# Performance work log

Measured on AMD Instinct MI355X. Metric: run time of the kernel, lower is better.

The kernel has to match this reference:

```python
import jax, jax.numpy as jnp
import numpy as np

NUM_CLASSES = 80
STRIDES = (8, 16, 32)


def _decode(p, stride):
    # p: [B, 5+C, H, W] raw head -> [B, HW, 5+C] decoded (xy in px, wh=exp*stride)
    B, C, H, W = p.shape
    ys, xs = jnp.meshgrid(jnp.arange(H), jnp.arange(W), indexing='ij')
    grid = jnp.stack([xs, ys], -1).reshape(H * W, 2).astype(p.dtype)
    out = p.reshape(B, C, H * W).transpose(0, 2, 1)
    xy = (out[..., :2] + grid) * stride
    wh = jnp.exp(out[..., 2:4]) * stride
    out = jnp.concatenate([xy, wh, out[..., 4:]], -1)
    es = jnp.full((H * W,), float(stride), p.dtype)
    return out, grid[:, 0], grid[:, 1], es


def _pairwise_iou(gt, pr):
    # gt [G,4] cxcywh, pr [A,4] -> [G,A]
    gt_tl = gt[:, None, :2] - gt[:, None, 2:] * 0.5
    gt_br = gt[:, None, :2] + gt[:, None, 2:] * 0.5
    pr_tl = pr[None, :, :2] - pr[None, :, 2:] * 0.5
    pr_br = pr[None, :, :2] + pr[None, :, 2:] * 0.5
    tl = jnp.maximum(gt_tl, pr_tl)
    br = jnp.minimum(gt_br, pr_br)
    en = jnp.all(tl < br, -1).astype(gt.dtype)
    inter = jnp.prod(br - tl, -1) * en
    a_gt = jnp.prod(gt[:, 2:], -1)[:, None]
    a_pr = jnp.prod(pr[:, 2:], -1)[None, :]
    return inter / (a_gt + a_pr - inter + 1e-16)


def _assign(gt_boxes, gt_cls, bbox, clsp, objp, xg, yg, es):
    # SimOTA assignment for one image (all fixed-shape; non-candidate anchors
    # are masked out via huge cost instead of boolean gather).
    G = gt_boxes.shape[0]
    xc = (xg + 0.5) * es  # [A] anchor centers
    yc = (yg + 0.5) * es
    gl = gt_boxes[:, 0:1] - 0.5 * gt_boxes[:, 2:3]
    gr = gt_boxes[:, 0:1] + 0.5 * gt_boxes[:, 2:3]
    gt_ = gt_boxes[:, 1:2] - 0.5 * gt_boxes[:, 3:4]
    gb = gt_boxes[:, 1:2] + 0.5 * gt_boxes[:, 3:4]
    in_box = (xc[None] > gl) & (xc[None] < gr) & (yc[None] > gt_) & (yc[None] < gb)  # [G,A]
    r = 2.5 * es[None]
    in_ctr = ((xc[None] > gt_boxes[:, 0:1] - r) & (xc[None] < gt_boxes[:, 0:1] + r)
              & (yc[None] > gt_boxes[:, 1:2] - r) & (yc[None] < gt_boxes[:, 1:2] + r))
    fg_cand = jnp.any(in_box, 0) | jnp.any(in_ctr, 0)  # [A]
    in_both = in_box & in_ctr  # [G,A]

    ious = _pairwise_iou(gt_boxes, bbox)  # [G,A]
    ious_m = jnp.where(fg_cand[None, :], ious, 0.0)
    iou_cost = -jnp.log(ious_m + 1e-8)

    # pairwise cls BCE cost: bce(sqrt(sigmoid(cls)*sigmoid(obj)), onehot(gt)).sum(-1)
    p = jnp.sqrt(jax.nn.sigmoid(clsp) * jax.nn.sigmoid(objp[:, None]))  # [A,C]
    lp = jnp.maximum(jnp.log(p), -100.0)
    l1p = jnp.maximum(jnp.log1p(-p), -100.0)
    t = jax.nn.one_hot(gt_cls, NUM_CLASSES, dtype=p.dtype)  # [G,C]
    cls_cost = -(jnp.einsum('ac,gc->ga', lp - l1p, t) + jnp.sum(l1p, -1)[None, :])

    cost = (cls_cost + 3.0 * iou_cost
            + 1e5 * (~in_both).astype(p.dtype)
            + 1e9 * (~fg_cand)[None, :].astype(p.dtype))

    # dynamic-k: k_g = clamp(sum(top10 ious), min=1)
    topk_ious, _ = jax.lax.top_k(ious_m, 10)
    dyn_k = jnp.clip(topk_ious.sum(-1).astype(jnp.int32), 1, None)  # [G]
    rank = jnp.argsort(jnp.argsort(cost, axis=1), axis=1)  # rank of each anchor per gt
    matching = (rank < dyn_k[:, None]) & fg_cand[None, :]  # [G,A]
    # resolve anchors matched to multiple gts: keep min-cost gt
    multi = matching.sum(0) > 1
    best = jnp.argmin(cost, 0)
    matching = jnp.where(multi[None, :], jnp.arange(G)[:, None] == best[None, :], matching)

    fg = jnp.any(matching, 0)  # [A]
    matched_gt = jnp.argmax(matching, 0)  # [A]
    pred_iou = jnp.sum(matching * ious, 0)  # [A]
    matched_cls = gt_cls[matched_gt]
    return fg, matched_gt, pred_iou, matched_cls


def _giou_loss(b, g):
    tl = jnp.maximum(b[..., :2] - b[..., 2:] * 0.5, g[..., :2] - g[..., 2:] * 0.5)
    br = jnp.minimum(b[..., :2] + b[..., 2:] * 0.5, g[..., :2] + g[..., 2:] * 0.5)
    area_b = jnp.prod(b[..., 2:], -1)
    area_g = jnp.prod(g[..., 2:], -1)
    en = jnp.all(tl < br, -1).astype(b.dtype)
    inter = jnp.prod(br - tl, -1) * en
    union = area_b + area_g - inter
    iou = inter / (union + 1e-16)
    ctl = jnp.minimum(b[..., :2] - b[..., 2:] * 0.5, g[..., :2] - g[..., 2:] * 0.5)
    cbr = jnp.maximum(b[..., :2] + b[..., 2:] * 0.5, g[..., :2] + g[..., 2:] * 0.5)
    area_c = jnp.maximum(jnp.prod(cbr - ctl, -1), 1e-16)
    giou = iou - (area_c - union) / area_c
    return 1.0 - jnp.clip(giou, -1.0, 1.0)


def _bce_logits(x, t):
    return jnp.maximum(x, 0.0) - x * t + jnp.log1p(jnp.exp(-jnp.abs(x)))


def _forward(p8, p16, p32, labels):
    outs, xo, yo, eo = [], [], [], []
    for p, s in zip((p8, p16, p32), STRIDES):
        o, x, y, e = _decode(p, s)
        outs.append(o); xo.append(x); yo.append(y); eo.append(e)
    outputs = jnp.concatenate(outs, 1)  # [B, A, 5+C]
    xg = jnp.concatenate(xo); yg = jnp.concatenate(yo); es = jnp.concatenate(eo)

    bbox = outputs[..., :4]
    obj = outputs[..., 4]
    cls = outputs[..., 5:]
    gt_boxes = labels[..., :4]
    gt_cls = labels[..., 4].astype(jnp.int32)

    # assignment runs under no_grad in torch
    det = jax.lax.stop_gradient(outputs)
    fg, matched_gt, pred_iou, matched_cls = jax.vmap(
        lambda gb, gc, o: _assign(gb, gc, o[..., :4], o[..., 5:], o[..., 4], xg, yg, es)
    )(gt_boxes, gt_cls, det)

    fgf = fg.astype(outputs.dtype)  # [B,A]
    reg_t = jnp.take_along_axis(gt_boxes, matched_gt[..., None], axis=1)  # [B,A,4]
    cls_t = (jax.nn.one_hot(matched_cls, NUM_CLASSES, dtype=outputs.dtype)
             * pred_iou[..., None] * fgf[..., None])

    loss_iou = jnp.sum(_giou_loss(bbox, reg_t) * fgf)
    loss_obj = jnp.sum(_bce_logits(obj, fgf))
    loss_cls = jnp.sum(_bce_logits(cls, cls_t) * fgf[..., None])
    num_fg = jnp.maximum(jnp.sum(fgf), 1.0)
    return (5.0 * loss_iou + loss_obj + loss_cls) / num_fg


def setup_inputs() -> dict:
    key = jax.random.key(0)
    k1, k2, k3, k4, k5, k6 = jax.random.split(key, 6)
    B, NGT = 32, 20
    p8 = jax.random.normal(k1, (B, 5 + NUM_CLASSES, 80, 80), dtype=jnp.float32)
    p16 = jax.random.normal(k2, (B, 5 + NUM_CLASSES, 40, 40), dtype=jnp.float32)
    p32 = jax.random.normal(k3, (B, 5 + NUM_CLASSES, 20, 20), dtype=jnp.float32)
    cxy = jax.random.uniform(k4, (B, NGT, 2), dtype=jnp.float32, minval=32.0, maxval=608.0)
    wh = jax.random.uniform(k5, (B, NGT, 2), dtype=jnp.float32, minval=16.0, maxval=128.0)
    cls = jax.random.randint(k6, (B, NGT, 1), 0, NUM_CLASSES).astype(jnp.float32)
    labels = jnp.concatenate([cxy, wh, cls], -1)
    return {"p8": p8, "p16": p16, "p32": p32, "labels": labels}


def reference(p8, p16, p32, labels):
    return _forward(p8, p16, p32, labels)
```

## Files before the change

kernel.cpp:

```cpp
#include <hip/hip_runtime.h>
#include <cstdint>
#include <cstddef>

#define NA 8400
#define NAP 8448
#define NB 32
#define NG 20
#define NCL 80
#define NBLK 33

__device__ __forceinline__ float frcp(float x) { return __builtin_amdgcn_rcpf(x); }
__device__ __forceinline__ float bce0(float x) {
  return fmaxf(x, 0.0f) + __logf(1.0f + __expf(-fabsf(x)));
}

__device__ __forceinline__ void anchor_info(int a, const float* p8, const float* p16,
                                            const float* p32, int b, const float*& base,
                                            int& hw, int& HW, int& xg, int& yg, float& fs) {
  if (a < 6400)      { hw = a;        HW = 6400; xg = hw % 80; yg = hw / 80; fs = 8.f;
                       base = p8  + (size_t)b * 85 * 6400; }
  else if (a < 8000) { hw = a - 6400; HW = 1600; xg = hw % 40; yg = hw / 40; fs = 16.f;
                       base = p16 + (size_t)b * 85 * 1600; }
  else               { hw = a - 8000; HW = 400;  xg = hw % 20; yg = hw / 20; fs = 32.f;
                       base = p32 + (size_t)b * 85 * 400; }
}

__device__ __forceinline__ float iou_raw(float gx, float gy, float gw, float gh, float4 p) {
  float gtlx = gx - gw * 0.5f, gtly = gy - gh * 0.5f;
  float gbrx = gx + gw * 0.5f, gbry = gy + gh * 0.5f;
  float ptlx = p.x - p.z * 0.5f, ptly = p.y - p.w * 0.5f;
  float pbrx = p.x + p.z * 0.5f, pbry = p.y + p.w * 0.5f;
  float tlx = fmaxf(gtlx, ptlx), tly = fmaxf(gtly, ptly);
  float brx = fminf(gbrx, pbrx), bry = fminf(gbry, pbry);
  float inter = ((tlx < brx) && (tly < bry)) ? (brx - tlx) * (bry - tly) : 0.0f;
  float ag = gw * gh, ap = p.z * p.w;
  return inter * frcp(ag + ap - inter + 1e-16f);
}

__device__ __forceinline__ float giou_loss(float4 bb, float gx, float gy, float gw, float gh) {
  float btlx = bb.x - bb.z * 0.5f, btly = bb.y - bb.w * 0.5f;
  float bbrx = bb.x + bb.z * 0.5f, bbry = bb.y + bb.w * 0.5f;
  float gtlx = gx - gw * 0.5f, gtly = gy - gh * 0.5f;
  float gbrx = gx + gw * 0.5f, gbry = gy + gh * 0.5f;
  float tlx = fmaxf(btlx, gtlx), tly = fmaxf(btly, gtly);
  float brx = fminf(bbrx, gbrx), bry = fminf(bbry, gbry);
  float area_b = bb.z * bb.w, area_g = gw * gh;
  float inter = ((tlx < brx) && (tly < bry)) ? (brx - tlx) * (bry - tly) : 0.0f;
  float uni = area_b + area_g - inter;
  float iou = inter / (uni + 1e-16f);
  float ctlx = fminf(btlx, gtlx), ctly = fminf(btly, gtly);
  float cbrx = fmaxf(bbrx, gbrx), cbry = fmaxf(bbry, gbry);
  float area_c = fmaxf((cbrx - ctlx) * (cbry - ctly), 1e-16f);
  float giou = iou - (area_c - uni) / area_c;
  giou = fminf(fmaxf(giou, -1.0f), 1.0f);
  return 1.0f - giou;
}

__global__ __launch_bounds__(256) void k1(const float* __restrict__ p8,
                                          const float* __restrict__ p16,
                                          const float* __restrict__ p32,
                                          const float* __restrict__ labels,
                                          int* __restrict__ n_fg_cnt,
                                          int* __restrict__ fg_list,
                                          unsigned int* __restrict__ am_c,
                                          float4* __restrict__ bbox_c,
                                          float* __restrict__ lso_c,
                                          unsigned int* __restrict__ match_c,
                                          float* __restrict__ blk_obj) {
  __shared__ float s_gt[NG * 4];
  __shared__ unsigned int s_wcnt[4];
  __shared__ float s_part[4];
  __shared__ unsigned int s_base;
  int blk = blockIdx.x, b = blockIdx.y, tid = threadIdx.x, lane = tid & 63, wid = tid >> 6;

  if (tid < NG) {
    s_gt[tid * 4 + 0] = labels[((size_t)b * NG + tid) * 5 + 0];
    s_gt[tid * 4 + 1] = labels[((size_t)b * NG + tid) * 5 + 1];
    s_gt[tid * 4 + 2] = labels[((size_t)b * NG + tid) * 5 + 2];
    s_gt[tid * 4 + 3] = labels[((size_t)b * NG + tid) * 5 + 3];
  }
  __syncthreads();

  int a = blk * 256 + tid;
  match_c[(size_t)b * NAP + a] = 0u;

  bool fg = false;
  unsigned int msk = 0u;
  float bce_obj = 0.0f, obj = 0.0f;
  const float* base = nullptr; int hw = 0, HW = 0, xg = 0, yg = 0; float fs = 8.f;
  if (a < NA) {
    anchor_info(a, p8, p16, p32, b, base, hw, HW, xg, yg, fs);
    obj = base[4 * HW + hw];
    bce_obj = bce0(obj);
    float xc = ((float)xg + 0.5f) * fs;
    float yc = ((float)yg + 0.5f) * fs;
    float r = 2.5f * fs;
#pragma unroll
    for (int g = 0; g < NG; ++g) {
      float gx = s_gt[g * 4 + 0], gy = s_gt[g * 4 + 1];
      float gw = s_gt[g * 4 + 2], gh = s_gt[g * 4 + 3];
      bool inb = (xc > gx - 0.5f * gw) && (xc < gx + 0.5f * gw) &&
                 (yc > gy - 0.5f * gh) && (yc < gy + 0.5f * gh);
      bool inc = (xc > gx - r) && (xc < gx + r) && (yc > gy - r) && (yc < gy + r);
      fg = fg || inb || inc;
      if (inb && inc) msk |= (1u << g);
    }
  }

  unsigned long long bm = __ballot(fg);
#pragma unroll
  for (int off = 32; off; off >>= 1) bce_obj += __shfl_down(bce_obj, off, 64);
  if (lane == 0) { s_wcnt[wid] = (unsigned int)__popcll(bm); s_part[wid] = bce_obj; }
  __syncthreads();
  if (tid == 0) {
    unsigned int cnt = s_wcnt[0] + s_wcnt[1] + s_wcnt[2] + s_wcnt[3];
    s_base = cnt ? (unsigned int)atomicAdd(&n_fg_cnt[b], (int)cnt) : 0u;
    blk_obj[b * NBLK + blk] = s_part[0] + s_part[1] + s_part[2] + s_part[3];
  }
  __syncthreads();

  if (!fg) return;
  unsigned int pos = s_base;
  for (int w = 0; w < wid; ++w) pos += s_wcnt[w];
  pos += (unsigned int)__popcll(bm & ((1ull << lane) - 1ull));
  size_t bo = (size_t)b * NAP;
  int ci = (int)pos;
  fg_list[bo + ci] = a;
  am_c[bo + ci] = msk;

  float v0 = base[hw];
  float v1 = base[HW + hw];
  float v2 = base[2 * HW + hw];
  float v3 = base[3 * HW + hw];
  bbox_c[bo + ci] = make_float4((v0 + (float)xg) * fs, (v1 + (float)yg) * fs,
                                __expf(v2) * fs, __expf(v3) * fs);
  float uo = __logf(1.0f + __expf(-fabsf(obj)));
  lso_c[bo + ci] = fminf(obj, 0.0f) - uo;
}

__global__ __launch_bounds__(256) void k23(const float* __restrict__ p8,
                                           const float* __restrict__ p16,
                                           const float* __restrict__ p32,
                                           const float* __restrict__ labels,
                                           const int* __restrict__ fg_list,
                                           const int* __restrict__ n_fg,
                                           const float* __restrict__ lso_c,
                                           const unsigned int* __restrict__ am_c,
                                           const float4* __restrict__ bbox_c,
                                           float* __restrict__ sb_c,
                                           float* __restrict__ cost_tbl,
                                           float* __restrict__ iou_tbl) {
  __shared__ float s_gt[NG * 4];
  __shared__ int   s_gcls[NG];
  __shared__ float s_sl[8][33];
  __shared__ float s_sb[8][33];
  __shared__ float s_slr[32];
  int b = blockIdx.y, tid = threadIdx.x;
  int part = tid >> 5, cl = tid & 31;

  if (tid < NG) {
    s_gt[tid * 4 + 0] = labels[((size_t)b * NG + tid) * 5 + 0];
    s_gt[tid * 4 + 1] = labels[((size_t)b * NG + tid) * 5 + 1];
    s_gt[tid * 4 + 2] = labels[((size_t)b * NG + tid) * 5 + 2];
    s_gt[tid * 4 + 3] = labels[((size_t)b * NG + tid) * 5 + 3];
    s_gcls[tid] = (int)labels[((size_t)b * NG + tid) * 5 + 4];
  }
  __syncthreads();

  int n = n_fg[b];
  size_t bo = (size_t)b * NAP;

  for (int base_ci = blockIdx.x * 32; base_ci < n; base_ci += gridDim.x * 32) {
    int ci = base_ci + cl;
    bool act = ci < n;
    const float* base = nullptr; int hw = 0, HW = 0, xg, yg; float fs;
    float lso = 0.0f, sl = 0.0f, sb = 0.0f;
    if (act) {
      int a = fg_list[bo + ci];
      lso = lso_c[bo + ci];
      anchor_info(a, p8, p16, p32, b, base, hw, HW, xg, yg, fs);
      const float* cb = base + (size_t)(5 + part * 10) * HW + hw;
      float xs[10];
#pragma unroll
      for (int j = 0; j < 10; ++j) xs[j] = cb[(size_t)j * HW];
#pragma unroll
      for (int j = 0; j < 10; ++j) {
        float x = xs[j];
        float u = __logf(1.0f + __expf(-fabsf(x)));
        sb += fmaxf(x, 0.0f) + u;
        float lsx = fminf(x, 0.0f) - u;
        float lpr = 0.5f * (lsx + lso);
        float p   = __expf(lpr);
        sl += fmaxf(__logf(1.0f - p), -100.0f);
      }
    }
    s_sl[part][cl] = sl;
    s_sb[part][cl] = sb;
    __syncthreads();
    if (tid < 32) {
      float tsl = 0.0f, tsb = 0.0f;
#pragma unroll
      for (int q = 0; q < 8; ++q) { tsl += s_sl[q][tid]; tsb += s_sb[q][tid]; }
      s_slr[tid] = tsl;
      if (base_ci + tid < n) sb_c[bo + base_ci + tid] = tsb;
    }
    __syncthreads();
    if (act) {
      float slr = s_slr[cl];
      unsigned int am = am_c[bo + ci];
      float4 pb = bbox_c[bo + ci];
#pragma unroll
      for (int gg = 0; gg < 3; ++gg) {
        int g = part + (gg << 3);
        if (g < NG) {
          int cg = s_gcls[g];
          float x = base[(size_t)(5 + cg) * HW + hw];
          float u = __logf(1.0f + __expf(-fabsf(x)));
          float lsx = fminf(x, 0.0f) - u;
          float lpr = 0.5f * (lsx + lso);
          float p   = __expf(lpr);
          float l1p = fmaxf(__logf(1.0f - p), -100.0f);
          float wv  = fmaxf(lpr, -100.0f) - l1p;
          float iou = iou_raw(s_gt[g * 4 + 0], s_gt[g * 4 + 1],
                              s_gt[g * 4 + 2], s_gt[g * 4 + 3], pb);
          float cst = -(wv + slr) - 3.0f * __logf(iou + 1e-8f);
          if (!((am >> g) & 1u)) cst += 100000.0f;
          size_t row = ((size_t)b * NG + g) * NAP;
          cost_tbl[row + ci] = cst;
          iou_tbl[row + ci]  = iou;
        }
      }
    }
    __syncthreads();
  }
}

__global__ __launch_bounds__(256) void kBCD(const float* __restrict__ p8,
                                            const float* __restrict__ p16,
                                            const float* __restrict__ p32,
                                            const float* __restrict__ labels,
                                            const float* __restrict__ cost_tbl,
                                            const float* __restrict__ iou_tbl,
                                            const int* __restrict__ n_fg,
                                            unsigned int* __restrict__ match_c,
                                            const int* __restrict__ fg_list,
                                            const float4* __restrict__ bbox_c,
                                            const float* __restrict__ sb_c,
                                            const float* __restrict__ blk_obj,
                                            float* __restrict__ accum,
                                            int* __restrict__ done_g,
                                            int* __restrict__ done_img,
                                            float* __restrict__ out) {
  __shared__ float s_wt[4 * 10];
  __shared__ float s_wc[4 * 10];
  __shared__ int   s_wi[4 * 10];
  __shared__ int   s_flag;
  __shared__ float s_gt[NG * 5];
  __shared__ float s_red[16];

  int g = blockIdx.x, b = blockIdx.y, tid = threadIdx.x;
  int lane = tid & 63, wid = tid >> 6;
  int n = n_fg[b];
  size_t bo = (size_t)b * NAP;
  const float* __restrict__ cg = cost_tbl + ((size_t)b * NG + g) * NAP;
  const float* __restrict__ ig = iou_tbl  + ((size_t)b * NG + g) * NAP;

  float t10[10];
  float c10v[10];
  int   c10i[10];
#pragma unroll
  for (int j = 0; j < 10; ++j) { t10[j] = 0.0f; c10v[j] = 3.4e38f; c10i[j] = 0x7fffffff; }

  for (int ci = tid; ci < n; ci += 256) {
    float iou = ig[ci];
    float cst = cg[ci];
    if (iou > t10[9]) {
      t10[9] = iou;
#pragma unroll
      for (int q = 9; q > 0; --q) {
        if (t10[q] > t10[q - 1]) { float t = t10[q]; t10[q] = t10[q - 1]; t10[q - 1] = t; }
        else break;
      }
    }
    if (cst < c10v[9] || (cst == c10v[9] && ci < c10i[9])) {
      c10v[9] = cst; c10i[9] = ci;
#pragma unroll
      for (int q = 9; q > 0; --q) {
        if (c10v[q] < c10v[q - 1] ||
            (c10v[q] == c10v[q - 1] && c10i[q] < c10i[q - 1])) {
          float tv = c10v[q]; c10v[q] = c10v[q - 1]; c10v[q - 1] = tv;
          int   ti = c10i[q]; c10i[q] = c10i[q - 1]; c10i[q - 1] = ti;
        } else break;
      }
    }
  }

  for (int r = 0; r < 10; ++r) {
    float v = t10[0];
    float bv = v;
    float cv = c10v[0]; int cix = c10i[0];
    float cbv = cv;     int cbi = cix;
#pragma unroll
    for (int off = 32; off; off >>= 1) {
      bv = fmaxf(bv, __shfl_down(bv, off, 64));
      float ov = __shfl_down(cbv, off, 64);
      int   oi = __shfl_down(cbi, off, 64);
      if (ov < cbv || (ov == cbv && oi < cbi)) { cbv = ov; cbi = oi; }
    }
    bv  = __shfl(bv, 0, 64);
    cbv = __shfl(cbv, 0, 64);
    cbi = __shfl(cbi, 0, 64);
    unsigned long long won = __ballot(v == bv);
    if (lane == __ffsll(won) - 1) {
#pragma unroll
      for (int q = 0; q < 9; ++q) t10[q] = t10[q + 1];
      t10[9] = -1.0f;
    }
    if (cv == cbv && cix == cbi) {
#pragma unroll
      for (int q = 0; q < 9; ++q) { c10v[q] = c10v[q + 1]; c10i[q] = c10i[q + 1]; }
      c10v[9] = 3.4e38f; c10i[9] = 0x7fffffff;
    }
    if (lane == 0) {
      s_wt[wid * 10 + r] = bv;
      s_wc[wid * 10 + r] = cbv;
      s_wi[wid * 10 + r] = cbi;
    }
  }
  __syncthreads();

  if (tid == 0) {
    int p0 = 0, p1 = 0, p2 = 0, p3 = 0;
    float s = 0.0f;
    for (int r = 0; r < 10; ++r) {
      float v0 = (p0 < 10) ? s_wt[p0]      : -2.0f;
      float v1 = (p1 < 10) ? s_wt[10 + p1] : -2.0f;
      float v2 = (p2 < 10) ? s_wt[20 + p2] : -2.0f;
      float v3 = (p3 < 10) ? s_wt[30 + p3] : -2.0f;
      float m = fmaxf(fmaxf(v0, v1), fmaxf(v2, v3));
      s += m;
      if (m == v0) ++p0; else if (m == v1) ++p1; else if (m == v2) ++p2; else ++p3;
    }
    int k = (int)s;
    if (k < 1) k = 1;
    int q[4] = {0, 0, 0, 0};
    for (int it = 0; it < k; ++it) {
      float bv = 3.3e38f; int bi = 0x7fffffff; int sel = -1;
#pragma unroll
      for (int w = 0; w < 4; ++w) {
        if (q[w] < 10) {
          float v = s_wc[w * 10 + q[w]];
          int   i = s_wi[w * 10 + q[w]];
          if (v < bv || (v == bv && i < bi)) { bv = v; bi = i; sel = w; }
        }
      }
      if (sel < 0 || bv >= 1e37f) break;
      atomicOr(&match_c[bo + bi], 1u << g);
      ++q[sel];
    }
    __threadfence();
    s_flag = (atomicAdd(&done_g[b], 1) == NG - 1) ? 1 : 0;
  }
  __syncthreads();
  if (!s_flag) return;

  if (tid < NG * 5) s_gt[tid] = labels[(size_t)b * NG * 5 + tid];
  __syncthreads();

  float li = 0.0f, oe = 0.0f, lc = 0.0f, nf = 0.0f;
  for (int ci = tid; ci < n; ci += 256) {
    unsigned int m = atomicOr(&match_c[bo + ci], 0u);
    if (m == 0u) continue;
    int mg;
    if (m & (m - 1)) {
      float bestc = 3.4e38f; mg = 0;
#pragma unroll 4
      for (int gq = 0; gq < NG; ++gq) {
        float cst = cost_tbl[((size_t)b * NG + gq) * NAP + ci];
        if (cst < bestc) { bestc = cst; mg = gq; }
      }
    } else {
      mg = __ffs(m) - 1;
    }
    int a = fg_list[bo + ci];
    const float* base; int hw, HW, xg, yg; float fs;
    anchor_info(a, p8, p16, p32, b, base, hw, HW, xg, yg, fs);
    float4 pb = bbox_c[bo + ci];
    float gx = s_gt[mg * 5], gy = s_gt[mg * 5 + 1];
    float gw = s_gt[mg * 5 + 2], gh = s_gt[mg * 5 + 3];
    int cgq = (int)s_gt[mg * 5 + 4];
    float piou = iou_tbl[((size_t)b * NG + mg) * NAP + ci];
    li += giou_loss(pb, gx, gy, gw, gh);
    float xcls = base[(size_t)(5 + cgq) * HW + hw];
    lc += sb_c[bo + ci] - xcls * piou;
    oe += base[4 * HW + hw];
    nf += 1.0f;
  }

  float vals[4] = {li, oe, lc, nf};
#pragma unroll
  for (int q2 = 0; q2 < 4; ++q2) {
#pragma unroll
    for (int off = 32; off; off >>= 1) vals[q2] += __shfl_down(vals[q2], off, 64);
  }
  if ((tid & 63) == 0) {
    int w = tid >> 6;
    s_red[w * 4 + 0] = vals[0];
    s_red[w * 4 + 1] = vals[1];
    s_red[w * 4 + 2] = vals[2];
    s_red[w * 4 + 3] = vals[3];
  }
  __syncthreads();
  if (tid < 4) {
    const int slot[4] = {0, 2, 3, 4};
    float s = s_red[tid] + s_red[4 + tid] + s_red[8 + tid] + s_red[12 + tid];
    atomicAdd(&accum[slot[tid]], s);
  }

  if (tid == 0) {
    __threadfence();
    s_flag = (atomicAdd(done_img, 1) == NB - 1) ? 1 : 0;
  }
  __syncthreads();
  if (!s_flag) return;

  float s = 0.0f;
  for (int i = tid; i < NB * NBLK; i += 256) s += blk_obj[i];
#pragma unroll
  for (int off = 32; off; off >>= 1) s += __shfl_down(s, off, 64);
  if ((tid & 63) == 0) s_red[tid >> 6] = s;
  __syncthreads();
  if (tid == 0) {
    float obj_base = s_red[0] + s_red[1] + s_red[2] + s_red[3];
    float loss_iou = atomicAdd(&accum[0], 0.0f);
    float oex      = atomicAdd(&accum[2], 0.0f);
    float loss_cls = atomicAdd(&accum[3], 0.0f);
    float num_fg   = atomicAdd(&accum[4], 0.0f);
    float loss_obj = obj_base - oex;
    out[0] = (5.0f * loss_iou + loss_obj + loss_cls) / fmaxf(num_fg, 1.0f);
  }
}

extern "C" void kernel_launch(void* const* d_in, const int* in_sizes, int n_in,
                              void* d_out, int out_size, void* d_ws, size_t ws_size,
                              hipStream_t stream) {
  const float* p8     = (const float*)d_in[0];
  const float* p16    = (const float*)d_in[1];
  const float* p32    = (const float*)d_in[2];
  const float* labels = (const float*)d_in[3];
  float* out = (float*)d_out;

  const size_t BAP = (size_t)NB * NAP;
  char* w = (char*)d_ws;
  float4*       bbox_c   = (float4*)w;
  float*        cost_tbl = (float*)(w + BAP * 16);
  float*        iou_tbl  = cost_tbl + (size_t)NB * NG * NAP;
  char*         w2       = (char*)(iou_tbl + (size_t)NB * NG * NAP);
  int*          fg_list  = (int*)(w2);
  unsigned int* match_c  = (unsigned int*)(w2 + BAP * 4);
  float*        sb_c     = (float*)(w2 + BAP * 8);
  float*        lso_c    = (float*)(w2 + BAP * 12);
  unsigned int* am_c     = (unsigned int*)(w2 + BAP * 16);
  char*         w3       = w2 + BAP * 20;
  int*          n_fg     = (int*)w3;
  float*        accum    = (float*)(w3 + 128);
  int*          done_g   = (int*)(w3 + 256);
  int*          done_img = (int*)(w3 + 384);
  float*        blk_obj  = (float*)(w3 + 512);

  hipMemsetAsync(w3, 0, 512, stream);

  k1<<<dim3(NBLK, NB), dim3(256), 0, stream>>>(p8, p16, p32, labels, n_fg, fg_list, am_c,
                                               bbox_c, lso_c, match_c, blk_obj);
  k23<<<dim3(NBLK, NB), dim3(256), 0, stream>>>(p8, p16, p32, labels, fg_list, n_fg, lso_c,
                                                am_c, bbox_c, sb_c, cost_tbl, iou_tbl);
  kBCD<<<dim3(NG, NB), dim3(256), 0, stream>>>(p8, p16, p32, labels, cost_tbl, iou_tbl,
                                               n_fg, match_c, fg_list, bbox_c, sb_c,
                                               blk_obj, accum, done_g, done_img, out);
}
```

Baseline: 183.5 us.

## Split SimOTA top-k matching into partitioned kernels and interleave cost/iou tables

New measurement: 207.4 us. 13.1% more time.

```diff
diff --git a/kernel.cpp b/kernel.cpp
--- a/kernel.cpp
+++ b/kernel.cpp
@@ -8,6 +8,7 @@
 #define NG 20
 #define NCL 80
 #define NBLK 33
+#define PSPL 4
 
 __device__ __forceinline__ float frcp(float x) { return __builtin_amdgcn_rcpf(x); }
 __device__ __forceinline__ float bce0(float x) {
@@ -148,8 +149,7 @@
                                            const unsigned int* __restrict__ am_c,
                                            const float4* __restrict__ bbox_c,
                                            float* __restrict__ sb_c,
-                                           float* __restrict__ cost_tbl,
-                                           float* __restrict__ iou_tbl) {
+                                           float2* __restrict__ ct_tbl) {
   __shared__ float s_gt[NG * 4];
   __shared__ int   s_gcls[NG];
   __shared__ float s_sl[8][33];
@@ -225,9 +225,7 @@
                               s_gt[g * 4 + 2], s_gt[g * 4 + 3], pb);
           float cst = -(wv + slr) - 3.0f * __logf(iou + 1e-8f);
           if (!((am >> g) & 1u)) cst += 100000.0f;
-          size_t row = ((size_t)b * NG + g) * NAP;
-          cost_tbl[row + ci] = cst;
-          iou_tbl[row + ci]  = iou;
+          ct_tbl[((size_t)b * NG + g) * NAP + ci] = make_float2(cst, iou);
         }
       }
     }
@@ -235,35 +233,18 @@
   }
 }
 
-__global__ __launch_bounds__(256) void kBCD(const float* __restrict__ p8,
-                                            const float* __restrict__ p16,
-                                            const float* __restrict__ p32,
-                                            const float* __restrict__ labels,
-                                            const float* __restrict__ cost_tbl,
-                                            const float* __restrict__ iou_tbl,
-                                            const int* __restrict__ n_fg,
-                                            unsigned int* __restrict__ match_c,
-                                            const int* __restrict__ fg_list,
-                                            const float4* __restrict__ bbox_c,
-                                            const float* __restrict__ sb_c,
-                                            const float* __restrict__ blk_obj,
-                                            float* __restrict__ accum,
-                                            int* __restrict__ done_g,
-                                            int* __restrict__ done_img,
-                                            float* __restrict__ out) {
+__global__ __launch_bounds__(256) void kBC(const float2* __restrict__ ct_tbl,
+                                           const int* __restrict__ n_fg,
+                                           float* __restrict__ scr_iou,
+                                           float* __restrict__ scr_cst,
+                                           int* __restrict__ scr_ci) {
   __shared__ float s_wt[4 * 10];
   __shared__ float s_wc[4 * 10];
   __shared__ int   s_wi[4 * 10];
-  __shared__ int   s_flag;
-  __shared__ float s_gt[NG * 5];
-  __shared__ float s_red[16];
-
-  int g = blockIdx.x, b = blockIdx.y, tid = threadIdx.x;
-  int lane = tid & 63, wid = tid >> 6;
+  int p = blockIdx.x, g = blockIdx.y, b = blockIdx.z;
+  int tid = threadIdx.x, lane = tid & 63, wid = tid >> 6;
   int n = n_fg[b];
-  size_t bo = (size_t)b * NAP;
-  const float* __restrict__ cg = cost_tbl + ((size_t)b * NG + g) * NAP;
-  const float* __restrict__ ig = iou_tbl  + ((size_t)b * NG + g) * NAP;
+  const float2* __restrict__ row = ct_tbl + ((size_t)b * NG + g) * NAP;
 
   float t10[10];
   float c10v[10];
@@ -271,9 +252,9 @@
 #pragma unroll
   for (int j = 0; j < 10; ++j) { t10[j] = 0.0f; c10v[j] = 3.4e38f; c10i[j] = 0x7fffffff; }
 
-  for (int ci = tid; ci < n; ci += 256) {
-    float iou = ig[ci];
-    float cst = cg[ci];
+  for (int ci = p * 256 + tid; ci < n; ci += PSPL * 256) {
+    float2 e = row[ci];
+    float cst = e.x, iou = e.y;
     if (iou > t10[9]) {
       t10[9] = iou;
 #pragma unroll
@@ -330,71 +311,138 @@
   __syncthreads();
 
   if (tid == 0) {
+    int obase = (((b * NG + g) * PSPL) + p) * 10;
     int p0 = 0, p1 = 0, p2 = 0, p3 = 0;
-    float s = 0.0f;
     for (int r = 0; r < 10; ++r) {
       float v0 = (p0 < 10) ? s_wt[p0]      : -2.0f;
       float v1 = (p1 < 10) ? s_wt[10 + p1] : -2.0f;
       float v2 = (p2 < 10) ? s_wt[20 + p2] : -2.0f;
       float v3 = (p3 < 10) ? s_wt[30 + p3] : -2.0f;
       float m = fmaxf(fmaxf(v0, v1), fmaxf(v2, v3));
-      s += m;
+      scr_iou[obase + r] = m;
       if (m == v0) ++p0; else if (m == v1) ++p1; else if (m == v2) ++p2; else ++p3;
     }
-    int k = (int)s;
-    if (k < 1) k = 1;
     int q[4] = {0, 0, 0, 0};
-    for (int it = 0; it < k; ++it) {
-      float bv = 3.3e38f; int bi = 0x7fffffff; int sel = -1;
+    for (int r = 0; r < 10; ++r) {
+      float bv = 0.0f; int bi = 0; int sel = -1;
 #pragma unroll
       for (int w = 0; w < 4; ++w) {
         if (q[w] < 10) {
           float v = s_wc[w * 10 + q[w]];
           int   i = s_wi[w * 10 + q[w]];
-          if (v < bv || (v == bv && i < bi)) { bv = v; bi = i; sel = w; }
+          if (sel < 0 || v < bv || (v == bv && i < bi)) { bv = v; bi = i; sel = w; }
         }
       }
-      if (sel < 0 || bv >= 1e37f) break;
-      atomicOr(&match_c[bo + bi], 1u << g);
+      scr_cst[obase + r] = bv;
+      scr_ci[obase + r]  = bi;
       ++q[sel];
     }
-    __threadfence();
-    s_flag = (atomicAdd(&done_g[b], 1) == NG - 1) ? 1 : 0;
-  }
-  __syncthreads();
-  if (!s_flag) return;
+  }
+}
+
+__global__ __launch_bounds__(64) void kM(const float* __restrict__ scr_iou,
+                                         const float* __restrict__ scr_cst,
+                                         const int* __restrict__ scr_ci,
+                                         unsigned int* __restrict__ match_c) {
+  int g = blockIdx.x, b = blockIdx.y, lane = threadIdx.x;
+  int bg = b * NG + g;
+  float v;
+  float cv; int cix;
+  if (lane < PSPL * 10) {
+    v   = scr_iou[bg * (PSPL * 10) + lane];
+    cv  = scr_cst[bg * (PSPL * 10) + lane];
+    cix = scr_ci [bg * (PSPL * 10) + lane];
+  } else {
+    v = -1.0f; cv = 3.4e38f; cix = 0x7fffffff;
+  }
+
+  float s = 0.0f;
+  for (int r = 0; r < 10; ++r) {
+    float bv = v;
+#pragma unroll
+    for (int off = 32; off; off >>= 1) bv = fmaxf(bv, __shfl_down(bv, off, 64));
+    bv = __shfl(bv, 0, 64);
+    s += bv;
+    unsigned long long won = __ballot(v == bv);
+    if (lane == __ffsll(won) - 1) v = -1.0f;
+  }
+  int k = (int)s;
+  if (k < 1) k = 1;
+
+  size_t bo = (size_t)b * NAP;
+  for (int it = 0; it < k; ++it) {
+    float cbv = cv; int cbi = cix;
+#pragma unroll
+    for (int off = 32; off; off >>= 1) {
+      float ov = __shfl_down(cbv, off, 64);
+      int   oi = __shfl_down(cbi, off, 64);
+      if (ov < cbv || (ov == cbv && oi < cbi)) { cbv = ov; cbi = oi; }
+    }
+    cbv = __shfl(cbv, 0, 64);
+    cbi = __shfl(cbi, 0, 64);
+    if (cbv >= 1e37f) break;
+    unsigned long long won = __ballot(cv == cbv && cix == cbi);
+    if (lane == __ffsll(won) - 1) {
+      atomicOr(&match_c[bo + cbi], 1u << g);
+      cv = 3.4e38f; cix = 0x7fffffff;
+    }
+  }
+}
+
+__global__ __launch_bounds__(256) void kD(const float* __restrict__ p8,
+                                          const float* __restrict__ p16,
+                                          const float* __restrict__ p32,
+                                          const float* __restrict__ labels,
+                                          const float2* __restrict__ ct_tbl,
+                                          const int* __restrict__ n_fg,
+                                          const unsigned int* __restrict__ match_c,
+                                          const int* __restrict__ fg_list,
+                                          const float4* __restrict__ bbox_c,
+                                          const float* __restrict__ sb_c,
+                                          const float* __restrict__ blk_obj,
+                                          float* __restrict__ accum,
+                                          int* __restrict__ done,
+                                          float* __restrict__ out) {
+  __shared__ float s_gt[NG * 5];
+  __shared__ float s_red[16];
+  __shared__ int s_flag;
+  int b = blockIdx.y, tid = threadIdx.x;
+  int n = n_fg[b];
+  size_t bo = (size_t)b * NAP;
 
   if (tid < NG * 5) s_gt[tid] = labels[(size_t)b * NG * 5 + tid];
   __syncthreads();
 
   float li = 0.0f, oe = 0.0f, lc = 0.0f, nf = 0.0f;
-  for (int ci = tid; ci < n; ci += 256) {
-    unsigned int m = atomicOr(&match_c[bo + ci], 0u);
-    if (m == 0u) continue;
-    int mg;
-    if (m & (m - 1)) {
-      float bestc = 3.4e38f; mg = 0;
+  int ci = blockIdx.x * 256 + tid;
+  if (ci < n) {
+    unsigned int m = match_c[bo + ci];
+    if (m != 0u) {
+      int mg;
+      if (m & (m - 1)) {
+        float bestc = 3.4e38f; mg = 0;
 #pragma unroll 4
-      for (int gq = 0; gq < NG; ++gq) {
-        float cst = cost_tbl[((size_t)b * NG + gq) * NAP + ci];
-        if (cst < bestc) { bestc = cst; mg = gq; }
+        for (int gq = 0; gq < NG; ++gq) {
+          float cst = ct_tbl[((size_t)b * NG + gq) * NAP + ci].x;
+          if (cst < bestc) { bestc = cst; mg = gq; }
+        }
+      } else {
+        mg = __ffs(m) - 1;
       }
-    } else {
-      mg = __ffs(m) - 1;
-    }
-    int a = fg_list[bo + ci];
-    const float* base; int hw, HW, xg, yg; float fs;
-    anchor_info(a, p8, p16, p32, b, base, hw, HW, xg, yg, fs);
-    float4 pb = bbox_c[bo + ci];
-    float gx = s_gt[mg * 5], gy = s_gt[mg * 5 + 1];
-    float gw = s_gt[mg * 5 + 2], gh = s_gt[mg * 5 + 3];
-    int cgq = (int)s_gt[mg * 5 + 4];
-    float piou = iou_tbl[((size_t)b * NG + mg) * NAP + ci];
-    li += giou_loss(pb, gx, gy, gw, gh);
-    float xcls = base[(size_t)(5 + cgq) * HW + hw];
-    lc += sb_c[bo + ci] - xcls * piou;
-    oe += base[4 * HW + hw];
-    nf += 1.0f;
+      int a = fg_list[bo + ci];
+      const float* base; int hw, HW, xg, yg; float fs;
+      anchor_info(a, p8, p16, p32, b, base, hw, HW, xg, yg, fs);
+      float4 pb = bbox_c[bo + ci];
+      float gx = s_gt[mg * 5], gy = s_gt[mg * 5 + 1];
+      float gw = s_gt[mg * 5 + 2], gh = s_gt[mg * 5 + 3];
+      int cgq = (int)s_gt[mg * 5 + 4];
+      float piou = ct_tbl[((size_t)b * NG + mg) * NAP + ci].y;
+      li = giou_loss(pb, gx, gy, gw, gh);
+      float xcls = base[(size_t)(5 + cgq) * HW + hw];
+      lc = sb_c[bo + ci] - xcls * piou;
+      oe = base[4 * HW + hw];
+      nf = 1.0f;
+    }
   }
 
   float vals[4] = {li, oe, lc, nf};
@@ -403,7 +451,8 @@
 #pragma unroll
     for (int off = 32; off; off >>= 1) vals[q2] += __shfl_down(vals[q2], off, 64);
   }
-  if ((tid & 63) == 0) {
+  int lane = tid & 63;
+  if (lane == 0) {
     int w = tid >> 6;
     s_red[w * 4 + 0] = vals[0];
     s_red[w * 4 + 1] = vals[1];
@@ -414,12 +463,13 @@
   if (tid < 4) {
     const int slot[4] = {0, 2, 3, 4};
     float s = s_red[tid] + s_red[4 + tid] + s_red[8 + tid] + s_red[12 + tid];
-    atomicAdd(&accum[slot[tid]], s);
-  }
+    if (s != 0.0f) atomicAdd(&accum[slot[tid]], s);
+  }
+  __syncthreads();
 
   if (tid == 0) {
     __threadfence();
-    s_flag = (atomicAdd(done_img, 1) == NB - 1) ? 1 : 0;
+    s_flag = (atomicAdd(done, 1) == NBLK * NB - 1) ? 1 : 0;
   }
   __syncthreads();
   if (!s_flag) return;
@@ -453,9 +503,8 @@
   const size_t BAP = (size_t)NB * NAP;
   char* w = (char*)d_ws;
   float4*       bbox_c   = (float4*)w;
-  float*        cost_tbl = (float*)(w + BAP * 16);
-  float*        iou_tbl  = cost_tbl + (size_t)NB * NG * NAP;
-  char*         w2       = (char*)(iou_tbl + (size_t)NB * NG * NAP);
+  float2*       ct_tbl   = (float2*)(w + BAP * 16);
+  char*         w2       = (char*)ct_tbl + (size_t)NB * NG * NAP * 8;
   int*          fg_list  = (int*)(w2);
   unsigned int* match_c  = (unsigned int*)(w2 + BAP * 4);
   float*        sb_c     = (float*)(w2 + BAP * 8);
@@ -464,17 +513,22 @@
   char*         w3       = w2 + BAP * 20;
   int*          n_fg     = (int*)w3;
   float*        accum    = (float*)(w3 + 128);
-  int*          done_g   = (int*)(w3 + 256);
-  int*          done_img = (int*)(w3 + 384);
+  int*          done     = (int*)(w3 + 384);
   float*        blk_obj  = (float*)(w3 + 512);
+  char*         scr      = w3 + 8192;
+  float*        scr_iou  = (float*)scr;
+  float*        scr_cst  = (float*)(scr + 102400);
+  int*          scr_ci   = (int*)  (scr + 204800);
 
   hipMemsetAsync(w3, 0, 512, stream);
 
-  k1<<<dim3(NBLK, NB), dim3(256), 0, stream>>>(p8, p16, p32, labels, n_fg, fg_list, am_c,
-                                               bbox_c, lso_c, match_c, blk_obj);
+  k1 <<<dim3(NBLK, NB), dim3(256), 0, stream>>>(p8, p16, p32, labels, n_fg, fg_list, am_c,
+                                                bbox_c, lso_c, match_c, blk_obj);
   k23<<<dim3(NBLK, NB), dim3(256), 0, stream>>>(p8, p16, p32, labels, fg_list, n_fg, lso_c,
-                                                am_c, bbox_c, sb_c, cost_tbl, iou_tbl);
-  kBCD<<<dim3(NG, NB), dim3(256), 0, stream>>>(p8, p16, p32, labels, cost_tbl, iou_tbl,
-                                               n_fg, match_c, fg_list, bbox_c, sb_c,
-                                               blk_obj, accum, done_g, done_img, out);
-}
+                                                am_c, bbox_c, sb_c, ct_tbl);
+  kBC<<<dim3(PSPL, NG, NB), dim3(256), 0, stream>>>(ct_tbl, n_fg, scr_iou, scr_cst, scr_ci);
+  kM <<<dim3(NG, NB), dim3(64), 0, stream>>>(scr_iou, scr_cst, scr_ci, match_c);
+  kD <<<dim3(NBLK, NB), dim3(256), 0, stream>>>(p8, p16, p32, labels, ct_tbl, n_fg, match_c,
+                                                fg_list, bbox_c, sb_c, blk_obj, accum,
+                                                done, out);
+}
```

## Fuse candidate and class-sum kernels; recompute per-GT cost instead of storing tables

Applied to the files above, without the earlier changes.

New measurement: 188.3 us. +2.6%, slower.

```diff
diff --git a/kernel.cpp b/kernel.cpp
--- a/kernel.cpp
+++ b/kernel.cpp
@@ -35,6 +35,24 @@
   float inter = ((tlx < brx) && (tly < bry)) ? (brx - tlx) * (bry - tly) : 0.0f;
   float ag = gw * gh, ap = p.z * p.w;
   return inter * frcp(ag + ap - inter + 1e-16f);
+}
+
+__device__ __forceinline__ float cost_for(float gx, float gy, float gw, float gh, int cg,
+                                          int g, unsigned int am, float lso, float slr,
+                                          const float* base, int hw, int HW, float4 pb,
+                                          float& iou_out) {
+  float x = base[(size_t)(5 + cg) * HW + hw];
+  float u = __logf(1.0f + __expf(-fabsf(x)));
+  float lsx = fminf(x, 0.0f) - u;
+  float lpr = 0.5f * (lsx + lso);
+  float p   = __expf(lpr);
+  float l1p = fmaxf(__logf(1.0f - p), -100.0f);
+  float wv  = fmaxf(lpr, -100.0f) - l1p;
+  float iou = iou_raw(gx, gy, gw, gh, pb);
+  iou_out = iou;
+  float cst = -(wv + slr) - 3.0f * __logf(iou + 1e-8f);
+  if (!((am >> g) & 1u)) cst += 100000.0f;
+  return cst;
 }
 
 __device__ __forceinline__ float giou_loss(float4 bb, float gx, float gy, float gw, float gh) {
@@ -56,22 +74,29 @@
   return 1.0f - giou;
 }
 
-__global__ __launch_bounds__(256) void k1(const float* __restrict__ p8,
+__global__ __launch_bounds__(256) void kA(const float* __restrict__ p8,
                                           const float* __restrict__ p16,
                                           const float* __restrict__ p32,
                                           const float* __restrict__ labels,
                                           int* __restrict__ n_fg_cnt,
-                                          int* __restrict__ fg_list,
-                                          unsigned int* __restrict__ am_c,
+                                          float4* __restrict__ meta_c,
                                           float4* __restrict__ bbox_c,
-                                          float* __restrict__ lso_c,
+                                          float* __restrict__ sb_c,
                                           unsigned int* __restrict__ match_c,
                                           float* __restrict__ blk_obj) {
   __shared__ float s_gt[NG * 4];
+  __shared__ int   s_a[256];
+  __shared__ unsigned int s_m[256];
+  __shared__ float s_lso[256];
+  __shared__ float s_sl[8][33];
+  __shared__ float s_sbv[8][33];
   __shared__ unsigned int s_wcnt[4];
   __shared__ float s_part[4];
   __shared__ unsigned int s_base;
+  __shared__ int s_cnt;
+
   int blk = blockIdx.x, b = blockIdx.y, tid = threadIdx.x, lane = tid & 63, wid = tid >> 6;
+  size_t bo = (size_t)b * NAP;
 
   if (tid < NG) {
     s_gt[tid * 4 + 0] = labels[((size_t)b * NG + tid) * 5 + 0];
@@ -82,8 +107,7 @@
   __syncthreads();
 
   int a = blk * 256 + tid;
-  match_c[(size_t)b * NAP + a] = 0u;
-
+  match_c[bo + a] = 0u;
   bool fg = false;
   unsigned int msk = 0u;
   float bce_obj = 0.0f, obj = 0.0f;
@@ -114,75 +138,44 @@
   __syncthreads();
   if (tid == 0) {
     unsigned int cnt = s_wcnt[0] + s_wcnt[1] + s_wcnt[2] + s_wcnt[3];
+    s_cnt = (int)cnt;
     s_base = cnt ? (unsigned int)atomicAdd(&n_fg_cnt[b], (int)cnt) : 0u;
     blk_obj[b * NBLK + blk] = s_part[0] + s_part[1] + s_part[2] + s_part[3];
   }
   __syncthreads();
 
-  if (!fg) return;
-  unsigned int pos = s_base;
-  for (int w = 0; w < wid; ++w) pos += s_wcnt[w];
-  pos += (unsigned int)__popcll(bm & ((1ull << lane) - 1ull));
-  size_t bo = (size_t)b * NAP;
-  int ci = (int)pos;
-  fg_list[bo + ci] = a;
-  am_c[bo + ci] = msk;
-
-  float v0 = base[hw];
-  float v1 = base[HW + hw];
-  float v2 = base[2 * HW + hw];
-  float v3 = base[3 * HW + hw];
-  bbox_c[bo + ci] = make_float4((v0 + (float)xg) * fs, (v1 + (float)yg) * fs,
-                                __expf(v2) * fs, __expf(v3) * fs);
-  float uo = __logf(1.0f + __expf(-fabsf(obj)));
-  lso_c[bo + ci] = fminf(obj, 0.0f) - uo;
-}
-
-__global__ __launch_bounds__(256) void k23(const float* __restrict__ p8,
-                                           const float* __restrict__ p16,
-                                           const float* __restrict__ p32,
-                                           const float* __restrict__ labels,
-                                           const int* __restrict__ fg_list,
-                                           const int* __restrict__ n_fg,
-                                           const float* __restrict__ lso_c,
-                                           const unsigned int* __restrict__ am_c,
-                                           const float4* __restrict__ bbox_c,
-                                           float* __restrict__ sb_c,
-                                           float* __restrict__ cost_tbl,
-                                           float* __restrict__ iou_tbl) {
-  __shared__ float s_gt[NG * 4];
-  __shared__ int   s_gcls[NG];
-  __shared__ float s_sl[8][33];
-  __shared__ float s_sb[8][33];
-  __shared__ float s_slr[32];
-  int b = blockIdx.y, tid = threadIdx.x;
+  if (fg) {
+    unsigned int li = 0;
+    for (int w = 0; w < wid; ++w) li += s_wcnt[w];
+    li += (unsigned int)__popcll(bm & ((1ull << lane) - 1ull));
+    float v0 = base[hw];
+    float v1 = base[HW + hw];
+    float v2 = base[2 * HW + hw];
+    float v3 = base[3 * HW + hw];
+    float4 bb4 = make_float4((v0 + (float)xg) * fs, (v1 + (float)yg) * fs,
+                             __expf(v2) * fs, __expf(v3) * fs);
+    float uo = __logf(1.0f + __expf(-fabsf(obj)));
+    float lso = fminf(obj, 0.0f) - uo;
+    s_a[li] = a; s_m[li] = msk; s_lso[li] = lso;
+    bbox_c[bo + s_base + li] = bb4;
+  }
+  __syncthreads();
+
+  int cnt = s_cnt;
   int part = tid >> 5, cl = tid & 31;
-
-  if (tid < NG) {
-    s_gt[tid * 4 + 0] = labels[((size_t)b * NG + tid) * 5 + 0];
-    s_gt[tid * 4 + 1] = labels[((size_t)b * NG + tid) * 5 + 1];
-    s_gt[tid * 4 + 2] = labels[((size_t)b * NG + tid) * 5 + 2];
-    s_gt[tid * 4 + 3] = labels[((size_t)b * NG + tid) * 5 + 3];
-    s_gcls[tid] = (int)labels[((size_t)b * NG + tid) * 5 + 4];
-  }
-  __syncthreads();
-
-  int n = n_fg[b];
-  size_t bo = (size_t)b * NAP;
-
-  for (int base_ci = blockIdx.x * 32; base_ci < n; base_ci += gridDim.x * 32) {
-    int ci = base_ci + cl;
-    bool act = ci < n;
-    const float* base = nullptr; int hw = 0, HW = 0, xg, yg; float fs;
-    float lso = 0.0f, sl = 0.0f, sb = 0.0f;
+  for (int t0 = 0; t0 < cnt; t0 += 32) {
+    int idx = t0 + cl;
+    bool act = idx < cnt;
+    float sl = 0.0f, sb = 0.0f;
     if (act) {
-      int a = fg_list[bo + ci];
-      lso = lso_c[bo + ci];
-      anchor_info(a, p8, p16, p32, b, base, hw, HW, xg, yg, fs);
-      const float* cb = base + (size_t)(5 + part * 10) * HW + hw;
+      int a2 = s_a[idx];
+      float lso = s_lso[idx];
+      const float* base2; int hw2, HW2, xg2, yg2; float fs2;
+      anchor_info(a2, p8, p16, p32, b, base2, hw2, HW2, xg2, yg2, fs2);
+      const float* cb = base2 + (size_t)(5 + part * 10) * HW2 + hw2;
       float xs[10];
 #pragma unroll
-      for (int j = 0; j < 10; ++j) xs[j] = cb[(size_t)j * HW];
+      for (int j = 0; j < 10; ++j) xs[j] = cb[(size_t)j * HW2];
 #pragma unroll
       for (int j = 0; j < 10; ++j) {
         float x = xs[j];
@@ -195,75 +188,57 @@
       }
     }
     s_sl[part][cl] = sl;
-    s_sb[part][cl] = sb;
+    s_sbv[part][cl] = sb;
     __syncthreads();
     if (tid < 32) {
-      float tsl = 0.0f, tsb = 0.0f;
-#pragma unroll
-      for (int q = 0; q < 8; ++q) { tsl += s_sl[q][tid]; tsb += s_sb[q][tid]; }
-      s_slr[tid] = tsl;
-      if (base_ci + tid < n) sb_c[bo + base_ci + tid] = tsb;
+      int idx2 = t0 + tid;
+      if (idx2 < cnt) {
+        float tsl = 0.0f, tsb = 0.0f;
+#pragma unroll
+        for (int q = 0; q < 8; ++q) { tsl += s_sl[q][tid]; tsb += s_sbv[q][tid]; }
+        int ci = (int)s_base + idx2;
+        sb_c[bo + ci] = tsb;
+        meta_c[bo + ci] = make_float4(s_lso[idx2], tsl,
+                                      __uint_as_float(s_m[idx2]),
+                                      __int_as_float(s_a[idx2]));
+      }
     }
     __syncthreads();
-    if (act) {
-      float slr = s_slr[cl];
-      unsigned int am = am_c[bo + ci];
-      float4 pb = bbox_c[bo + ci];
-#pragma unroll
-      for (int gg = 0; gg < 3; ++gg) {
-        int g = part + (gg << 3);
-        if (g < NG) {
-          int cg = s_gcls[g];
-          float x = base[(size_t)(5 + cg) * HW + hw];
-          float u = __logf(1.0f + __expf(-fabsf(x)));
-          float lsx = fminf(x, 0.0f) - u;
-          float lpr = 0.5f * (lsx + lso);
-          float p   = __expf(lpr);
-          float l1p = fmaxf(__logf(1.0f - p), -100.0f);
-          float wv  = fmaxf(lpr, -100.0f) - l1p;
-          float iou = iou_raw(s_gt[g * 4 + 0], s_gt[g * 4 + 1],
-                              s_gt[g * 4 + 2], s_gt[g * 4 + 3], pb);
-          float cst = -(wv + slr) - 3.0f * __logf(iou + 1e-8f);
-          if (!((am >> g) & 1u)) cst += 100000.0f;
-          size_t row = ((size_t)b * NG + g) * NAP;
-          cost_tbl[row + ci] = cst;
-          iou_tbl[row + ci]  = iou;
-        }
-      }
-    }
-    __syncthreads();
-  }
-}
-
-__global__ __launch_bounds__(256) void kBCD(const float* __restrict__ p8,
-                                            const float* __restrict__ p16,
-                                            const float* __restrict__ p32,
-                                            const float* __restrict__ labels,
-                                            const float* __restrict__ cost_tbl,
-                                            const float* __restrict__ iou_tbl,
-                                            const int* __restrict__ n_fg,
-                                            unsigned int* __restrict__ match_c,
-                                            const int* __restrict__ fg_list,
-                                            const float4* __restrict__ bbox_c,
-                                            const float* __restrict__ sb_c,
-                                            const float* __restrict__ blk_obj,
-                                            float* __restrict__ accum,
-                                            int* __restrict__ done_g,
-                                            int* __restrict__ done_img,
-                                            float* __restrict__ out) {
+  }
+}
+
+__global__ __launch_bounds__(256) void kBG(const float* __restrict__ p8,
+                                           const float* __restrict__ p16,
+                                           const float* __restrict__ p32,
+                                           const float* __restrict__ labels,
+                                           const int* __restrict__ n_fg,
+                                           const float4* __restrict__ meta_c,
+                                           const float4* __restrict__ bbox_c,
+                                           const float* __restrict__ sb_c,
+                                           unsigned int* __restrict__ match_c,
+                                           const float* __restrict__ blk_obj,
+                                           float* __restrict__ accum,
+                                           int* __restrict__ done_g,
+                                           int* __restrict__ done_img,
+                                           float* __restrict__ out) {
+  __shared__ float s_gt[NG * 5];
   __shared__ float s_wt[4 * 10];
   __shared__ float s_wc[4 * 10];
   __shared__ int   s_wi[4 * 10];
+  __shared__ float s_red[16];
   __shared__ int   s_flag;
-  __shared__ float s_gt[NG * 5];
-  __shared__ float s_red[16];
 
   int g = blockIdx.x, b = blockIdx.y, tid = threadIdx.x;
   int lane = tid & 63, wid = tid >> 6;
   int n = n_fg[b];
   size_t bo = (size_t)b * NAP;
-  const float* __restrict__ cg = cost_tbl + ((size_t)b * NG + g) * NAP;
-  const float* __restrict__ ig = iou_tbl  + ((size_t)b * NG + g) * NAP;
+
+  if (tid < NG * 5) s_gt[tid] = labels[(size_t)b * NG * 5 + tid];
+  __syncthreads();
+
+  float ggx = s_gt[g * 5], ggy = s_gt[g * 5 + 1];
+  float ggw = s_gt[g * 5 + 2], ggh = s_gt[g * 5 + 3];
+  int   gcg = (int)s_gt[g * 5 + 4];
 
   float t10[10];
   float c10v[10];
@@ -272,8 +247,15 @@
   for (int j = 0; j < 10; ++j) { t10[j] = 0.0f; c10v[j] = 3.4e38f; c10i[j] = 0x7fffffff; }
 
   for (int ci = tid; ci < n; ci += 256) {
-    float iou = ig[ci];
-    float cst = cg[ci];
+    float4 me = meta_c[bo + ci];
+    float lso = me.x, slr = me.y;
+    unsigned int am = __float_as_uint(me.z);
+    int a = __float_as_int(me.w);
+    const float* base; int hw, HW, xg, yg; float fs;
+    anchor_info(a, p8, p16, p32, b, base, hw, HW, xg, yg, fs);
+    float4 pb = bbox_c[bo + ci];
+    float iou;
+    float cst = cost_for(ggx, ggy, ggw, ggh, gcg, g, am, lso, slr, base, hw, HW, pb, iou);
     if (iou > t10[9]) {
       t10[9] = iou;
 #pragma unroll
@@ -364,32 +346,34 @@
   __syncthreads();
   if (!s_flag) return;
 
-  if (tid < NG * 5) s_gt[tid] = labels[(size_t)b * NG * 5 + tid];
-  __syncthreads();
-
   float li = 0.0f, oe = 0.0f, lc = 0.0f, nf = 0.0f;
   for (int ci = tid; ci < n; ci += 256) {
     unsigned int m = atomicOr(&match_c[bo + ci], 0u);
     if (m == 0u) continue;
+    float4 me = meta_c[bo + ci];
+    float lso = me.x, slr = me.y;
+    unsigned int am = __float_as_uint(me.z);
+    int a = __float_as_int(me.w);
+    const float* base; int hw, HW, xg, yg; float fs;
+    anchor_info(a, p8, p16, p32, b, base, hw, HW, xg, yg, fs);
+    float4 pb = bbox_c[bo + ci];
     int mg;
     if (m & (m - 1)) {
       float bestc = 3.4e38f; mg = 0;
-#pragma unroll 4
       for (int gq = 0; gq < NG; ++gq) {
-        float cst = cost_tbl[((size_t)b * NG + gq) * NAP + ci];
-        if (cst < bestc) { bestc = cst; mg = gq; }
+        float iouq;
+        float cq = cost_for(s_gt[gq * 5], s_gt[gq * 5 + 1], s_gt[gq * 5 + 2],
+                            s_gt[gq * 5 + 3], (int)s_gt[gq * 5 + 4], gq, am,
+                            lso, slr, base, hw, HW, pb, iouq);
+        if (cq < bestc) { bestc = cq; mg = gq; }
       }
     } else {
       mg = __ffs(m) - 1;
     }
-    int a = fg_list[bo + ci];
-    const float* base; int hw, HW, xg, yg; float fs;
-    anchor_info(a, p8, p16, p32, b, base, hw, HW, xg, yg, fs);
-    float4 pb = bbox_c[bo + ci];
     float gx = s_gt[mg * 5], gy = s_gt[mg * 5 + 1];
     float gw = s_gt[mg * 5 + 2], gh = s_gt[mg * 5 + 3];
     int cgq = (int)s_gt[mg * 5 + 4];
-    float piou = iou_tbl[((size_t)b * NG + mg) * NAP + ci];
+    float piou = iou_raw(gx, gy, gw, gh, pb);
     li += giou_loss(pb, gx, gy, gw, gh);
     float xcls = base[(size_t)(5 + cgq) * HW + hw];
     lc += sb_c[bo + ci] - xcls * piou;
@@ -403,12 +387,11 @@
 #pragma unroll
     for (int off = 32; off; off >>= 1) vals[q2] += __shfl_down(vals[q2], off, 64);
   }
-  if ((tid & 63) == 0) {
-    int w = tid >> 6;
-    s_red[w * 4 + 0] = vals[0];
-    s_red[w * 4 + 1] = vals[1];
-    s_red[w * 4 + 2] = vals[2];
-    s_red[w * 4 + 3] = vals[3];
+  if (lane == 0) {
+    s_red[wid * 4 + 0] = vals[0];
+    s_red[wid * 4 + 1] = vals[1];
+    s_red[wid * 4 + 2] = vals[2];
+    s_red[wid * 4 + 3] = vals[3];
   }
   __syncthreads();
   if (tid < 4) {
@@ -453,15 +436,11 @@
   const size_t BAP = (size_t)NB * NAP;
   char* w = (char*)d_ws;
   float4*       bbox_c   = (float4*)w;
-  float*        cost_tbl = (float*)(w + BAP * 16);
-  float*        iou_tbl  = cost_tbl + (size_t)NB * NG * NAP;
-  char*         w2       = (char*)(iou_tbl + (size_t)NB * NG * NAP);
-  int*          fg_list  = (int*)(w2);
+  float4*       meta_c   = (float4*)(w + BAP * 16);
+  char*         w2       = w + BAP * 32;
+  float*        sb_c     = (float*)(w2);
   unsigned int* match_c  = (unsigned int*)(w2 + BAP * 4);
-  float*        sb_c     = (float*)(w2 + BAP * 8);
-  float*        lso_c    = (float*)(w2 + BAP * 12);
-  unsigned int* am_c     = (unsigned int*)(w2 + BAP * 16);
-  char*         w3       = w2 + BAP * 20;
+  char*         w3       = w2 + BAP * 8;
   int*          n_fg     = (int*)w3;
   float*        accum    = (float*)(w3 + 128);
   int*          done_g   = (int*)(w3 + 256);
@@ -470,11 +449,9 @@
 
   hipMemsetAsync(w3, 0, 512, stream);
 
-  k1<<<dim3(NBLK, NB), dim3(256), 0, stream>>>(p8, p16, p32, labels, n_fg, fg_list, am_c,
-                                               bbox_c, lso_c, match_c, blk_obj);
-  k23<<<dim3(NBLK, NB), dim3(256), 0, stream>>>(p8, p16, p32, labels, fg_list, n_fg, lso_c,
-                                                am_c, bbox_c, sb_c, cost_tbl, iou_tbl);
-  kBCD<<<dim3(NG, NB), dim3(256), 0, stream>>>(p8, p16, p32, labels, cost_tbl, iou_tbl,
-                                               n_fg, match_c, fg_list, bbox_c, sb_c,
-                                               blk_obj, accum, done_g, done_img, out);
-}
+  kA <<<dim3(NBLK, NB), dim3(256), 0, stream>>>(p8, p16, p32, labels, n_fg, meta_c,
+                                                bbox_c, sb_c, match_c, blk_obj);
+  kBG<<<dim3(NG, NB), dim3(256), 0, stream>>>(p8, p16, p32, labels, n_fg, meta_c, bbox_c,
+                                              sb_c, match_c, blk_obj, accum, done_g,
+                                              done_img, out);
+}
```
